# Kernel optimization log

Hardware: AMD Instinct MI355X
Metric: run time of the kernel (lower is better)

Reference implementation:

```python
import jax, jax.numpy as jnp
import numpy as np

N_NODES = 100000
N_EDGES = 400000
N_GRAPHS = 2500
DIM = 128
F_IN = 78
N_LAYERS = 3
BN_EPS = 1e-5


def setup_inputs() -> dict:
    key = jax.random.key(0)
    ks = jax.random.split(key, 24)
    def lin(k, fi, fo):
        return jax.random.normal(k, (fi, fo), jnp.float32) / np.sqrt(fi)
    inp = {
        "x": jax.random.normal(ks[0], (N_NODES, F_IN), jnp.float32),
        "edge_index": jax.random.randint(ks[1], (2, N_EDGES), 0, N_NODES, jnp.int32),
        "batch": jnp.sort(jax.random.randint(ks[2], (N_NODES,), 0, N_GRAPHS, jnp.int32)),
        "num_graphs": N_GRAPHS,
        "gcn1_W": lin(ks[3], F_IN, DIM), "gcn1_b": jnp.zeros((DIM,), jnp.float32),
        "gcn2_W": lin(ks[4], DIM, DIM), "gcn2_b": jnp.zeros((DIM,), jnp.float32),
        "gin0_w1": lin(ks[5], F_IN, DIM), "gin0_b1": jnp.zeros((DIM,), jnp.float32),
        "gin0_w2": lin(ks[6], DIM, DIM), "gin0_b2": jnp.zeros((DIM,), jnp.float32),
        # layers 1..2 stacked (same 128->128 shapes)
        "gin_w1": jnp.stack([lin(ks[7], DIM, DIM), lin(ks[8], DIM, DIM)]),
        "gin_b1": jnp.zeros((2, DIM), jnp.float32),
        "gin_w2": jnp.stack([lin(ks[9], DIM, DIM), lin(ks[10], DIM, DIM)]),
        "gin_b2": jnp.zeros((2, DIM), jnp.float32),
        "bn_gamma": jnp.ones((N_LAYERS, DIM), jnp.float32),
        "bn_beta": jnp.zeros((N_LAYERS, DIM), jnp.float32),
    }
    return inp


def reference(x, edge_index, batch, num_graphs,
              gcn1_W, gcn1_b, gcn2_W, gcn2_b,
              gin0_w1, gin0_b1, gin0_w2, gin0_b2,
              gin_w1, gin_b1, gin_w2, gin_b2,
              bn_gamma, bn_beta):
    n = x.shape[0]
    src, dst = edge_index[0], edge_index[1]

    def gcn(h, W, b):
        # linear -> symmetric-normalized aggregation with self loops (PyG GCNConv)
        h = h @ W
        loop = jnp.arange(n, dtype=src.dtype)
        s = jnp.concatenate([src, loop])
        d = jnp.concatenate([dst, loop])
        deg = jax.ops.segment_sum(jnp.ones(s.shape[0], h.dtype), d, num_segments=n)
        dis = jax.lax.rsqrt(deg)  # deg >= 1 thanks to self loops
        norm = (dis[s] * dis[d])[:, None]
        return jax.ops.segment_sum(h[s] * norm, d, num_segments=n) + b

    def gin(h, w1, b1, w2, b2):
        # GINConv, eps=0: mlp(x + sum_{j->i} x_j)
        agg = jax.ops.segment_sum(h[src], dst, num_segments=n)
        z = jax.nn.relu((h + agg) @ w1 + b1)
        return z @ w2 + b2

    def bn(h, g, bt):
        mu = h.mean(0)
        var = ((h - mu) ** 2).mean(0)
        return (h - mu) * jax.lax.rsqrt(var + BN_EPS) * g + bt

    g1 = jax.nn.relu(gcn(x, gcn1_W, gcn1_b))
    g2 = jax.nn.relu(gcn(g1, gcn2_W, gcn2_b))
    g2a = g2 + g1
    g2m = g2 * g1

    h = x
    xs = []
    m = jnp.float32(1.0)
    e = jnp.float32(0.0)
    for i in range(N_LAYERS):
        if i == 0:
            h = gin(h, gin0_w1, gin0_b1, gin0_w2, gin0_b2)
        else:
            h = gin(h, gin_w1[i - 1], gin_b1[i - 1], gin_w2[i - 1], gin_b2[i - 1])
        h = bn(jax.nn.relu(h), bn_gamma[i], bn_beta[i])
        m = m * h
        e = e + h
        xs.append(h)

    rep = jnp.concatenate(xs + [m, e, g1, g2, g2a, g2m], axis=-1)  # [N, 9*DIM]
    return jax.ops.segment_max(rep, batch, num_segments=num_graphs)
```

## Files before the change

### kernel.cpp

```cpp
#include <hip/hip_runtime.h>
#include <math.h>

#define DIMC 128
#define FINC 78
#define REPW 1152
#define SCAN_TILE 1024

typedef __attribute__((ext_vector_type(8))) short short8x;
typedef __attribute__((ext_vector_type(4))) float f32x4;

__device__ inline float b2f(unsigned short u) {
    union { unsigned int i; float f; } v; v.i = ((unsigned int)u) << 16; return v.f;
}
__device__ inline unsigned short f2b(float f) {
    union { float f; unsigned int i; } v; v.f = f;
    unsigned int r = (v.i + 0x7FFFu + ((v.i >> 16) & 1u)) >> 16;
    return (unsigned short)r;
}
__device__ inline float pf2f(unsigned int u) {
    union { unsigned int i; float f; } hi, lo;
    hi.i = u & 0xFFFF0000u;
    lo.i = u << 16;
    return hi.f + lo.f;
}
__device__ inline unsigned int f2pf(float v) {
    unsigned short hi = f2b(v);
    unsigned short lo = f2b(v - b2f(hi));
    return ((unsigned int)hi << 16) | (unsigned int)lo;
}
__device__ inline void pfacc4(uint4 u, float* a) {
    a[0] += pf2f(u.x); a[1] += pf2f(u.y); a[2] += pf2f(u.z); a[3] += pf2f(u.w);
}


__global__ void k_fill_int(int* __restrict__ p, int v, int n) {
    int i = blockIdx.x * blockDim.x + threadIdx.x;
    if (i < n) p[i] = v;
}

__global__ void k_fill(float* __restrict__ p, float v, int n) {
    int i = blockIdx.x * blockDim.x + threadIdx.x;
    if (i < n) p[i] = v;
}

__global__ void k_count(const int* __restrict__ dst, int* __restrict__ cnt, int E) {
    int e = blockIdx.x * blockDim.x + threadIdx.x;
    if (e < E) atomicAdd(&cnt[dst[e]], 1);
}

__launch_bounds__(256)
__global__ void k_tilesum(const int* __restrict__ cnt, int* __restrict__ tileSum, int N) {
    __shared__ int red[256];
    int base = blockIdx.x * SCAN_TILE;
    int s = 0;
    for (int i = threadIdx.x; i < SCAN_TILE; i += 256) {
        int idx = base + i;
        if (idx < N) s += cnt[idx];
    }
    red[threadIdx.x] = s;
    __syncthreads();
    for (int d = 128; d > 0; d >>= 1) {
        if (threadIdx.x < d) red[threadIdx.x] += red[threadIdx.x + d];
        __syncthreads();
    }
    if (threadIdx.x == 0) tileSum[blockIdx.x] = red[0];
}

__launch_bounds__(256)
__global__ void k_tilescan(const int* __restrict__ tileSum, int* __restrict__ tileOff,
                           int* __restrict__ rowptr, int T, int N) {
    __shared__ int sh[256];
    int t = threadIdx.x;
    int orig = (t < T) ? tileSum[t] : 0;
    sh[t] = orig;
    __syncthreads();
    for (int d = 1; d < 256; d <<= 1) {
        int v = (t >= d) ? sh[t - d] : 0;
        __syncthreads();
        sh[t] += v;
        __syncthreads();
    }
    if (t < T) tileOff[t] = sh[t] - orig;
    if (t == 255) rowptr[N] = sh[255];
}

__launch_bounds__(256)
__global__ void k_tileemit(const int* __restrict__ cnt, const int* __restrict__ tileOff,
                           int* __restrict__ rowptr, int* __restrict__ cursor,
                           float* __restrict__ dis, int N) {
    __shared__ int sh[256];
    int t = threadIdx.x;
    int base = blockIdx.x * SCAN_TILE;
    int idx0 = base + t * 4;
    int v0 = 0, v1 = 0, v2 = 0, v3 = 0;
    if (idx0 + 3 < N) {
        int4 v = *(const int4*)(cnt + idx0);
        v0 = v.x; v1 = v.y; v2 = v.z; v3 = v.w;
    } else {
        if (idx0 + 0 < N) v0 = cnt[idx0 + 0];
        if (idx0 + 1 < N) v1 = cnt[idx0 + 1];
        if (idx0 + 2 < N) v2 = cnt[idx0 + 2];
        if (idx0 + 3 < N) v3 = cnt[idx0 + 3];
    }
    int s0 = v0, s1 = s0 + v1, s2 = s1 + v2, s3 = s2 + v3;
    sh[t] = s3;
    __syncthreads();
    for (int d = 1; d < 256; d <<= 1) {
        int v = (t >= d) ? sh[t - d] : 0;
        __syncthreads();
        sh[t] += v;
        __syncthreads();
    }
    int gbase = tileOff[blockIdx.x] + ((t == 0) ? 0 : sh[t - 1]);
    int ex[4] = {0, s0, s1, s2};
    int vv[4] = {v0, v1, v2, v3};
#pragma unroll
    for (int j = 0; j < 4; ++j) {
        int idx = idx0 + j;
        if (idx < N) {
            int r = gbase + ex[j];
            rowptr[idx] = r;
            cursor[idx] = r;
            dis[idx] = rsqrtf((float)vv[j] + 1.0f);
        }
    }
}

__global__ void k_scatter(const int* __restrict__ src, const int* __restrict__ dst,
                          int* __restrict__ cursor, int* __restrict__ col, int E) {
    int e = blockIdx.x * blockDim.x + threadIdx.x;
    if (e < E) {
        int pos = atomicAdd(&cursor[dst[e]], 1);
        col[pos] = src[e];
    }
}

__global__ void k_bounds(const int* __restrict__ batch, int* __restrict__ start, int N, int G) {
    int g = blockIdx.x * blockDim.x + threadIdx.x;
    if (g <= G) {
        int lo = 0, hi = N;
        while (lo < hi) { int mid = (lo + hi) >> 1; if (batch[mid] < g) lo = mid + 1; else hi = mid; }
        start[g] = lo;
    }
}


__global__ void k_cvt_x(const float* __restrict__ x, unsigned int* __restrict__ xpk, int N) {
    int i = blockIdx.x * blockDim.x + threadIdx.x;
    if (i < N * 96) {
        int n = i / 96, k = i - n * 96;
        float v = (k < FINC) ? x[(size_t)n * FINC + k] : 0.f;
        xpk[i] = f2pf(v);
    }
}

__global__ void k_cvt_w(const float* __restrict__ s0, const float* __restrict__ s1,
                        const float* __restrict__ s2, const float* __restrict__ s3,
                        const float* __restrict__ s4, const float* __restrict__ s5,
                        unsigned short* __restrict__ whi, unsigned short* __restrict__ wlo) {
    int my = blockIdx.y;
    const float* src; int Ksrc, KP; size_t dstoff;
    const size_t o96 = (size_t)128 * 96, o128 = (size_t)128 * 128;
    switch (my) {
        case 0: src = s0; Ksrc = 78;  KP = 96;  dstoff = 0; break;
        case 1: src = s1; Ksrc = 78;  KP = 96;  dstoff = o96; break;
        case 2: src = s2; Ksrc = 128; KP = 128; dstoff = 2 * o96; break;
        case 3: src = s3; Ksrc = 128; KP = 128; dstoff = 2 * o96 + o128; break;
        case 4: src = s4; Ksrc = 128; KP = 128; dstoff = 2 * o96 + 2 * o128; break;
        default: src = s5; Ksrc = 128; KP = 128; dstoff = 2 * o96 + 3 * o128; break;
    }
    int i = blockIdx.x * blockDim.x + threadIdx.x;
    if (i < 128 * KP) {
        int n = i / KP, k = i - n * KP;
        float v = (k < Ksrc) ? src[(size_t)k * DIMC + n] : 0.f;
        unsigned short hi = f2b(v);
        wlo[dstoff + i] = f2b(v - b2f(hi));
        whi[dstoff + i] = hi;
    }
}


__launch_bounds__(256)
__global__ void k_bn_w(const float* __restrict__ bnsum, const float* __restrict__ gamma,
                       const float* __restrict__ beta, const float* __restrict__ w1,
                       float* __restrict__ coef, unsigned short* __restrict__ whiO,
                       unsigned short* __restrict__ wloO, float* __restrict__ cbeta, float invN) {
    __shared__ float sS[128], sT[128], sC[256];
    int t = threadIdx.x;
    if (t < 128) {
        float mu  = bnsum[t] * invN;
        float var = bnsum[128 + t] * invN - mu * mu;
        float inv = rsqrtf(var + 1e-5f);
        float s = gamma[t] * inv;
        float sh = beta[t] - mu * s;
        coef[t] = s; coef[128 + t] = sh;
        sS[t] = s; sT[t] = sh;
    }
    __syncthreads();
    for (int i = t; i < 16384; i += 256) {
        int n = i >> 7, k = i & 127;
        float v = w1[(size_t)k * 128 + n] * sS[k];
        unsigned short hi = f2b(v);
        whiO[i] = hi;
        wloO[i] = f2b(v - b2f(hi));
    }
    int n = t & 127, half = t >> 7;
    float acc = 0.f;
    for (int k = half * 64; k < half * 64 + 64; ++k) acc = fmaf(sT[k], w1[(size_t)k * 128 + n], acc);
    sC[t] = acc;
    __syncthreads();
    if (t < 128) cbeta[t] = sC[t] + sC[t + 128];
}

__global__ void k_bn_coef(const float* __restrict__ bnsum, const float* __restrict__ gamma,
                          const float* __restrict__ beta, float* __restrict__ coef, float invN) {
    int c = threadIdx.x;
    float mu  = bnsum[c] * invN;
    float var = bnsum[128 + c] * invN - mu * mu;
    float inv = rsqrtf(var + 1e-5f);
    float s = gamma[c] * inv;
    coef[c] = s;
    coef[128 + c] = beta[c] - mu * s;
}


template<int KP>
__launch_bounds__(256)
__global__ void k_gemm_pf(const unsigned int* __restrict__ Apk,
                          const unsigned short* __restrict__ Whi,
                          const unsigned short* __restrict__ Wlo,
                          const float* __restrict__ bias,
                          const float* __restrict__ rowScale,
                          float* __restrict__ statsOut,
                          unsigned int* __restrict__ Cpk,
                          int N, int doRelu) {
    __shared__ unsigned short sAhi[4 * 66 * 8], sAlo[4 * 66 * 8];
    __shared__ unsigned short sBhi[4 * 130 * 8], sBlo[4 * 130 * 8];
    __shared__ float sStats[256];
    const int tid = threadIdx.x;
    const int row0 = blockIdx.x * 64;

    const int wave = tid >> 6;
    const int lane = tid & 63;
    const int lm = lane & 15, q = lane >> 4;
    const int wc = wave * 32;

    f32x4 acc[4][2];
#pragma unroll
    for (int a = 0; a < 4; ++a)
#pragma unroll
        for (int b = 0; b < 2; ++b) acc[a][b] = (f32x4){0.f, 0.f, 0.f, 0.f};

    for (int k0 = 0; k0 < KP; k0 += 32) {
        if (k0) __syncthreads();
        {
            int g = tid & 3, r = tid >> 2;
            int gr = row0 + r;
            uint4 h = make_uint4(0, 0, 0, 0), l = make_uint4(0, 0, 0, 0);
            if (gr < N) {
                const unsigned int* p = Apk + (size_t)gr * KP + k0 + g * 8;
                uint4 u0 = *(const uint4*)(p);
                uint4 u1 = *(const uint4*)(p + 4);
                h.x = (u0.x >> 16) | (u0.y & 0xFFFF0000u);
                l.x = (u0.x & 0xFFFFu) | (u0.y << 16);
                h.y = (u0.z >> 16) | (u0.w & 0xFFFF0000u);
                l.y = (u0.z & 0xFFFFu) | (u0.w << 16);
                h.z = (u1.x >> 16) | (u1.y & 0xFFFF0000u);
                l.z = (u1.x & 0xFFFFu) | (u1.y << 16);
                h.w = (u1.z >> 16) | (u1.w & 0xFFFF0000u);
                l.w = (u1.z & 0xFFFFu) | (u1.w << 16);
            }
            size_t la = ((size_t)g * 66 + r) * 8;
            *(uint4*)(sAhi + la) = h;
            *(uint4*)(sAlo + la) = l;
        }
        for (int s = tid; s < 512; s += 256) {
            int g = s & 3, n = s >> 2;
            size_t gb = (size_t)n * KP + k0 + g * 8;
            size_t la = ((size_t)g * 130 + n) * 8;
            *(uint4*)(sBhi + la) = *(const uint4*)(Whi + gb);
            *(uint4*)(sBlo + la) = *(const uint4*)(Wlo + gb);
        }
        __syncthreads();

        short8x ah[4], al[4], bh[2], bl[2];
#pragma unroll
        for (int rt = 0; rt < 4; ++rt) {
            size_t addr = ((size_t)q * 66 + rt * 16 + lm) * 8;
            ah[rt] = *(const short8x*)(sAhi + addr);
            al[rt] = *(const short8x*)(sAlo + addr);
        }
#pragma unroll
        for (int ct = 0; ct < 2; ++ct) {
            size_t addr = ((size_t)q * 130 + wc + ct * 16 + lm) * 8;
            bh[ct] = *(const short8x*)(sBhi + addr);
            bl[ct] = *(const short8x*)(sBlo + addr);
        }
#pragma unroll
        for (int rt = 0; rt < 4; ++rt)
#pragma unroll
            for (int ct = 0; ct < 2; ++ct) {
                acc[rt][ct] = __builtin_amdgcn_mfma_f32_16x16x32_bf16(ah[rt], bh[ct], acc[rt][ct], 0, 0, 0);
                acc[rt][ct] = __builtin_amdgcn_mfma_f32_16x16x32_bf16(ah[rt], bl[ct], acc[rt][ct], 0, 0, 0);
                acc[rt][ct] = __builtin_amdgcn_mfma_f32_16x16x32_bf16(al[rt], bh[ct], acc[rt][ct], 0, 0, 0);
            }
    }

    float cs[2] = {0.f, 0.f}, cq[2] = {0.f, 0.f};
#pragma unroll
    for (int rt = 0; rt < 4; ++rt) {
#pragma unroll
        for (int i = 0; i < 4; ++i) {
            int row = rt * 16 + q * 4 + i;
            int gr = row0 + row;
            if (gr < N) {
                float sc = rowScale ? rowScale[gr] : 1.f;
#pragma unroll
                for (int ct = 0; ct < 2; ++ct) {
                    int colg = wc + ct * 16 + lm;
                    float v = acc[rt][ct][i];
                    if (bias) v += bias[colg];
                    if (doRelu) v = fmaxf(v, 0.f);
                    v *= sc;
                    Cpk[(size_t)gr * DIMC + colg] = f2pf(v);
                    if (statsOut) { cs[ct] += v; cq[ct] = fmaf(v, v, cq[ct]); }
                }
            }
        }
    }
    if (statsOut) {
        sStats[tid] = 0.f;
        __syncthreads();
#pragma unroll
        for (int ct = 0; ct < 2; ++ct) {
            int colg = wc + ct * 16 + lm;
            atomicAdd(&sStats[colg], cs[ct]);
            atomicAdd(&sStats[128 + colg], cq[ct]);
        }
        __syncthreads();
        atomicAdd(&statsOut[tid], sStats[tid]);
    }
}


__global__ void k_gather_gcn_pf(const unsigned int* __restrict__ t, const int* __restrict__ rowptr,
                                const int* __restrict__ col, const float* __restrict__ dis,
                                const float* __restrict__ bias, unsigned int* __restrict__ out, int N) {
    int i = blockIdx.x * blockDim.x + threadIdx.x;
    int node = i >> 5, c4 = (i & 31) * 4;
    if (node >= N) return;
    int s = rowptr[node], e = rowptr[node + 1];
    float acc[4] = {0.f, 0.f, 0.f, 0.f};
    pfacc4(*(const uint4*)(t + (size_t)node * DIMC + c4), acc);
    int k = s;
    for (; k + 1 < e; k += 2) {
        uint4 v0 = *(const uint4*)(t + (size_t)col[k] * DIMC + c4);
        uint4 v1 = *(const uint4*)(t + (size_t)col[k + 1] * DIMC + c4);
        pfacc4(v0, acc);
        pfacc4(v1, acc);
    }
    if (k < e) pfacc4(*(const uint4*)(t + (size_t)col[k] * DIMC + c4), acc);
    float d = dis[node];
    uint4 r;
    r.x = f2pf(fmaxf(acc[0] * d + bias[c4 + 0], 0.f));
    r.y = f2pf(fmaxf(acc[1] * d + bias[c4 + 1], 0.f));
    r.z = f2pf(fmaxf(acc[2] * d + bias[c4 + 2], 0.f));
    r.w = f2pf(fmaxf(acc[3] * d + bias[c4 + 3], 0.f));
    *(uint4*)(out + (size_t)node * DIMC + c4) = r;
}

__global__ void k_gather_gin_pf(const unsigned int* __restrict__ t, const int* __restrict__ rowptr,
                                const int* __restrict__ col, const float* __restrict__ bias,
                                const float* __restrict__ cbeta, unsigned int* __restrict__ out, int N) {
    int i = blockIdx.x * blockDim.x + threadIdx.x;
    int node = i >> 5, c4 = (i & 31) * 4;
    if (node >= N) return;
    int s = rowptr[node], e = rowptr[node + 1];
    float acc[4] = {0.f, 0.f, 0.f, 0.f};
    pfacc4(*(const uint4*)(t + (size_t)node * DIMC + c4), acc);
    int k = s;
    for (; k + 1 < e; k += 2) {
        uint4 v0 = *(const uint4*)(t + (size_t)col[k] * DIMC + c4);
        uint4 v1 = *(const uint4*)(t + (size_t)col[k + 1] * DIMC + c4);
        pfacc4(v0, acc);
        pfacc4(v1, acc);
    }
    if (k < e) pfacc4(*(const uint4*)(t + (size_t)col[k] * DIMC + c4), acc);
    float deg1 = (float)(e - s + 1);
    uint4 r;
#pragma unroll
    for (int j = 0; j < 4; ++j) {
        float v = acc[j] + bias[c4 + j];
        if (cbeta) v = fmaf(deg1, cbeta[c4 + j], v);
        ((unsigned int*)&r)[j] = f2pf(fmaxf(v, 0.f));
    }
    *(uint4*)(out + (size_t)node * DIMC + c4) = r;
}


__global__ void k_segmax_gin_all(const unsigned int* __restrict__ h0, const unsigned int* __restrict__ h1,
                                 const unsigned int* __restrict__ h2, const float* __restrict__ coef,
                                 const int* __restrict__ start, float* __restrict__ out) {
    int g = blockIdx.x, c = threadIdx.x;
    float s0 = coef[c],       t0 = coef[128 + c];
    float s1 = coef[256 + c], t1 = coef[384 + c];
    float s2 = coef[512 + c], t2 = coef[640 + c];
    int s = start[g], e = start[g + 1];
    float m0 = -INFINITY, m1 = -INFINITY, m2 = -INFINITY, mm = -INFINITY, me = -INFINITY;
    for (int n = s; n < e; ++n) {
        size_t idx = (size_t)n * DIMC + c;
        float a0 = fmaf(pf2f(h0[idx]), s0, t0);
        float a1 = fmaf(pf2f(h1[idx]), s1, t1);
        float a2 = fmaf(pf2f(h2[idx]), s2, t2);
        m0 = fmaxf(m0, a0); m1 = fmaxf(m1, a1); m2 = fmaxf(m2, a2);
        mm = fmaxf(mm, a0 * a1 * a2);
        me = fmaxf(me, a0 + a1 + a2);
    }
    size_t o = (size_t)g * REPW + c;
    out[o]            = m0;
    out[o + 1 * DIMC] = m1;
    out[o + 2 * DIMC] = m2;
    out[o + 3 * DIMC] = mm;
    out[o + 4 * DIMC] = me;
}

__global__ void k_segmax_gcn(const unsigned int* __restrict__ G1, const unsigned int* __restrict__ G2,
                             const int* __restrict__ start, float* __restrict__ out) {
    int g = blockIdx.x, c = threadIdx.x;
    int s = start[g], e = start[g + 1];
    float m1 = -INFINITY, m2 = -INFINITY, ma = -INFINITY, mm = -INFINITY;
    for (int n = s; n < e; ++n) {
        size_t idx = (size_t)n * DIMC + c;
        float a = pf2f(G1[idx]);
        float b = pf2f(G2[idx]);
        m1 = fmaxf(m1, a); m2 = fmaxf(m2, b);
        ma = fmaxf(ma, a + b); mm = fmaxf(mm, a * b);
    }
    size_t o = (size_t)g * REPW + c;
    out[o + 5 * DIMC] = m1;
    out[o + 6 * DIMC] = m2;
    out[o + 7 * DIMC] = ma;
    out[o + 8 * DIMC] = mm;
}


extern "C" void kernel_launch(void* const* d_in, const int* in_sizes, int n_in,
                              void* d_out, int out_size, void* d_ws, size_t ws_size,
                              hipStream_t stream) {
    const float* x       = (const float*)d_in[0];
    const int*   ei      = (const int*)d_in[1];
    const int*   batch   = (const int*)d_in[2];
    const float* gcn1_W  = (const float*)d_in[4];
    const float* gcn1_b  = (const float*)d_in[5];
    const float* gcn2_W  = (const float*)d_in[6];
    const float* gcn2_b  = (const float*)d_in[7];
    const float* gin0_w1 = (const float*)d_in[8];
    const float* gin0_b1 = (const float*)d_in[9];
    const float* gin0_w2 = (const float*)d_in[10];
    const float* gin0_b2 = (const float*)d_in[11];
    const float* gin_w1  = (const float*)d_in[12];
    const float* gin_b1  = (const float*)d_in[13];
    const float* gin_w2  = (const float*)d_in[14];
    const float* gin_b2  = (const float*)d_in[15];
    const float* bn_g    = (const float*)d_in[16];
    const float* bn_b    = (const float*)d_in[17];
    float* out = (float*)d_out;

    const int N = in_sizes[0] / FINC;
    const int E = in_sizes[1] / 2;
    const int G = out_size / REPW;
    const int* srcv = ei;
    const int* dstv = ei + E;

    auto cdiv = [](long a, long b) { return (int)((a + b - 1) / b); };
    const int gemmGrid = cdiv(N, 64);

    char* ws = (char*)d_ws;
    size_t off = 0;
    auto alloc = [&](size_t bytes) { char* p = ws + off; off += (bytes + 255) & ~(size_t)255; return p; };
    int*   cnt     = (int*)alloc(N * 4);
    int*   rowptr  = (int*)alloc((N + 1) * 4);
    int*   cursor  = (int*)alloc(N * 4);
    int*   col     = (int*)alloc(E * 4);
    float* dis     = (float*)alloc(N * 4);
    float* bnsum   = (float*)alloc(768 * 4);
    float* coef    = (float*)alloc(768 * 4);
    float* cbeta   = (float*)alloc(128 * 4);
    int*   start   = (int*)alloc((G + 1) * 4);
    int*   tileSum = (int*)alloc(256 * 4);
    int*   tileOff = (int*)alloc(256 * 4);
    const size_t wtElems = 2 * (size_t)128 * 96 + 4 * (size_t)128 * 128;
    unsigned short* whi = (unsigned short*)alloc(wtElems * 2);
    unsigned short* wlo = (unsigned short*)alloc(wtElems * 2);
    unsigned short* w1shi = (unsigned short*)alloc((size_t)128 * 128 * 2);
    unsigned short* w1slo = (unsigned short*)alloc((size_t)128 * 128 * 2);
    const size_t P = (size_t)N * DIMC;
    unsigned int* tT = (unsigned int*)alloc(P * 4);
    unsigned int* z  = (unsigned int*)alloc(P * 4);
    unsigned int* h0 = (unsigned int*)alloc(P * 4);
    unsigned int* h1 = (unsigned int*)alloc(P * 4);
    unsigned int* h2 = (unsigned int*)alloc(P * 4);
    unsigned int* xpk = h2;
    (void)ws_size; (void)n_in;

    const size_t o96 = (size_t)128 * 96, o128 = (size_t)128 * 128;
    const size_t woff[6] = {0, o96, 2 * o96, 2 * o96 + o128, 2 * o96 + 2 * o128, 2 * o96 + 3 * o128};

    const int T = 256;
    const int gatherGrid = cdiv((long)N * 32, T);
    const int nTiles = cdiv(N, SCAN_TILE);
    const float invN = 1.0f / (float)N;

    k_fill_int<<<cdiv(N, T), T, 0, stream>>>(cnt, 0, N);
    k_count<<<cdiv(E, T), T, 0, stream>>>(dstv, cnt, E);
    k_tilesum<<<nTiles, T, 0, stream>>>(cnt, tileSum, N);
    k_tilescan<<<1, T, 0, stream>>>(tileSum, tileOff, rowptr, nTiles, N);
    k_tileemit<<<nTiles, T, 0, stream>>>(cnt, tileOff, rowptr, cursor, dis, N);
    k_scatter<<<cdiv(E, T), T, 0, stream>>>(srcv, dstv, cursor, col, E);
    k_bounds<<<cdiv(G + 1, T), T, 0, stream>>>(batch, start, N, G);
    k_fill<<<3, T, 0, stream>>>(bnsum, 0.f, 768);
    k_cvt_x<<<cdiv((long)N * 96, T), T, 0, stream>>>(x, xpk, N);
    {
        dim3 g(64, 6);
        k_cvt_w<<<g, T, 0, stream>>>(gcn1_W, gin0_w1, gcn2_W, gin0_w2,
                                     gin_w2, gin_w2 + o128, whi, wlo);
    }

    k_gemm_pf<96><<<gemmGrid, T, 0, stream>>>(xpk, whi + woff[0], wlo + woff[0],
                                              nullptr, dis, nullptr, tT, N, 0);
    k_gather_gcn_pf<<<gatherGrid, T, 0, stream>>>(tT, rowptr, col, dis, gcn1_b, h1, N);
    k_gemm_pf<128><<<gemmGrid, T, 0, stream>>>(h1, whi + woff[2], wlo + woff[2],
                                               nullptr, dis, nullptr, tT, N, 0);
    k_gather_gcn_pf<<<gatherGrid, T, 0, stream>>>(tT, rowptr, col, dis, gcn2_b, z, N);
    k_segmax_gcn<<<G, DIMC, 0, stream>>>(h1, z, start, out);

    k_gemm_pf<96><<<gemmGrid, T, 0, stream>>>(xpk, whi + woff[1], wlo + woff[1],
                                              nullptr, nullptr, nullptr, tT, N, 0);
    k_gather_gin_pf<<<gatherGrid, T, 0, stream>>>(tT, rowptr, col, gin0_b1, nullptr, z, N);
    k_gemm_pf<128><<<gemmGrid, T, 0, stream>>>(z, whi + woff[3], wlo + woff[3],
                                               gin0_b2, nullptr, bnsum, h0, N, 1);

    const unsigned int* hsrc[2] = {h0, h1};
    unsigned int* hdst[2] = {h1, h2};
    for (int L = 1; L <= 2; ++L) {
        k_bn_w<<<1, T, 0, stream>>>(bnsum + (L - 1) * 256, bn_g + (L - 1) * DIMC, bn_b + (L - 1) * DIMC,
                                    gin_w1 + (size_t)(L - 1) * o128, coef + (L - 1) * 256,
                                    w1shi, w1slo, cbeta, invN);
        k_gemm_pf<128><<<gemmGrid, T, 0, stream>>>(hsrc[L - 1], w1shi, w1slo,
                                                   nullptr, nullptr, nullptr, tT, N, 0);
        k_gather_gin_pf<<<gatherGrid, T, 0, stream>>>(tT, rowptr, col,
                                                      gin_b1 + (size_t)(L - 1) * DIMC, cbeta, z, N);
        k_gemm_pf<128><<<gemmGrid, T, 0, stream>>>(z, whi + woff[3 + L], wlo + woff[3 + L],
                                                   gin_b2 + (size_t)(L - 1) * DIMC, nullptr,
                                                   bnsum + L * 256, hdst[L - 1], N, 1);
    }
    k_bn_coef<<<1, DIMC, 0, stream>>>(bnsum + 512, bn_g + 2 * DIMC, bn_b + 2 * DIMC, coef + 512, invN);

    k_segmax_gin_all<<<G, DIMC, 0, stream>>>(h0, h1, h2, coef, start, out);
}
```

Measured before the change: 812.0 us.

## Prefetch all A chunks into registers and stage full weight matrix in LDS

The GEMM kernel now issues every global load for its A rows up front, holding them in registers, and copies the whole B (weight hi/lo) matrix into shared memory once before the K loop. Previously each 32-wide K chunk waited on its own global loads. The intent is to hide global memory latency and remove the per-chunk B reloads. In exchange it uses more registers and more shared memory (NG*130*8*2 shorts for B), which can lower occupancy.

```diff
diff --git a/kernel.cpp b/kernel.cpp
--- a/kernel.cpp
+++ b/kernel.cpp
@@ -234,8 +234,10 @@
                           float* __restrict__ statsOut,
                           unsigned int* __restrict__ Cpk,
                           int N, int doRelu) {
+    constexpr int NCH = KP / 32;
+    constexpr int NG  = KP / 8;
     __shared__ unsigned short sAhi[4 * 66 * 8], sAlo[4 * 66 * 8];
-    __shared__ unsigned short sBhi[4 * 130 * 8], sBlo[4 * 130 * 8];
+    __shared__ unsigned short sBhi[NG * 130 * 8], sBlo[NG * 130 * 8];
     __shared__ float sStats[256];
     const int tid = threadIdx.x;
     const int row0 = blockIdx.x * 64;
@@ -245,41 +247,51 @@
     const int lm = lane & 15, q = lane >> 4;
     const int wc = wave * 32;
 
+    const int ag = tid & 3, ar = tid >> 2;
+    const int agr = row0 + ar;
+    uint4 apre[2 * NCH];
+    if (agr < N) {
+        const unsigned int* p = Apk + (size_t)agr * KP + ag * 8;
+#pragma unroll
+        for (int c = 0; c < NCH; ++c) {
+            apre[2 * c]     = *(const uint4*)(p + c * 32);
+            apre[2 * c + 1] = *(const uint4*)(p + c * 32 + 4);
+        }
+    } else {
+#pragma unroll
+        for (int c = 0; c < 2 * NCH; ++c) apre[c] = make_uint4(0, 0, 0, 0);
+    }
+
+    for (int s = tid; s < NG * 128; s += 256) {
+        int g = s >> 7, n = s & 127;
+        size_t gb = (size_t)n * KP + g * 8;
+        size_t la = ((size_t)g * 130 + n) * 8;
+        *(uint4*)(sBhi + la) = *(const uint4*)(Whi + gb);
+        *(uint4*)(sBlo + la) = *(const uint4*)(Wlo + gb);
+    }
+
     f32x4 acc[4][2];
 #pragma unroll
     for (int a = 0; a < 4; ++a)
 #pragma unroll
         for (int b = 0; b < 2; ++b) acc[a][b] = (f32x4){0.f, 0.f, 0.f, 0.f};
 
-    for (int k0 = 0; k0 < KP; k0 += 32) {
-        if (k0) __syncthreads();
+#pragma unroll
+    for (int c = 0; c < NCH; ++c) {
         {
-            int g = tid & 3, r = tid >> 2;
-            int gr = row0 + r;
-            uint4 h = make_uint4(0, 0, 0, 0), l = make_uint4(0, 0, 0, 0);
-            if (gr < N) {
-                const unsigned int* p = Apk + (size_t)gr * KP + k0 + g * 8;
-                uint4 u0 = *(const uint4*)(p);
-                uint4 u1 = *(const uint4*)(p + 4);
-                h.x = (u0.x >> 16) | (u0.y & 0xFFFF0000u);
-                l.x = (u0.x & 0xFFFFu) | (u0.y << 16);
-                h.y = (u0.z >> 16) | (u0.w & 0xFFFF0000u);
-                l.y = (u0.z & 0xFFFFu) | (u0.w << 16);
-                h.z = (u1.x >> 16) | (u1.y & 0xFFFF0000u);
-                l.z = (u1.x & 0xFFFFu) | (u1.y << 16);
-                h.w = (u1.z >> 16) | (u1.w & 0xFFFF0000u);
-                l.w = (u1.z & 0xFFFFu) | (u1.w << 16);
-            }
-            size_t la = ((size_t)g * 66 + r) * 8;
+            uint4 u0 = apre[2 * c], u1 = apre[2 * c + 1];
+            uint4 h, l;
+            h.x = (u0.x >> 16) | (u0.y & 0xFFFF0000u);
+            l.x = (u0.x & 0xFFFFu) | (u0.y << 16);
+            h.y = (u0.z >> 16) | (u0.w & 0xFFFF0000u);
+            l.y = (u0.z & 0xFFFFu) | (u0.w << 16);
+            h.z = (u1.x >> 16) | (u1.y & 0xFFFF0000u);
+            l.z = (u1.x & 0xFFFFu) | (u1.y << 16);
+            h.w = (u1.z >> 16) | (u1.w & 0xFFFF0000u);
+            l.w = (u1.z & 0xFFFFu) | (u1.w << 16);
+            size_t la = ((size_t)ag * 66 + ar) * 8;
             *(uint4*)(sAhi + la) = h;
             *(uint4*)(sAlo + la) = l;
-        }
-        for (int s = tid; s < 512; s += 256) {
-            int g = s & 3, n = s >> 2;
-            size_t gb = (size_t)n * KP + k0 + g * 8;
-            size_t la = ((size_t)g * 130 + n) * 8;
-            *(uint4*)(sBhi + la) = *(const uint4*)(Whi + gb);
-            *(uint4*)(sBlo + la) = *(const uint4*)(Wlo + gb);
         }
         __syncthreads();
 
@@ -292,7 +304,7 @@
         }
 #pragma unroll
         for (int ct = 0; ct < 2; ++ct) {
-            size_t addr = ((size_t)q * 130 + wc + ct * 16 + lm) * 8;
+            size_t addr = ((size_t)(c * 4 + q) * 130 + wc + ct * 16 + lm) * 8;
             bh[ct] = *(const short8x*)(sBhi + addr);
             bl[ct] = *(const short8x*)(sBlo + addr);
         }
@@ -304,6 +316,7 @@
                 acc[rt][ct] = __builtin_amdgcn_mfma_f32_16x16x32_bf16(ah[rt], bl[ct], acc[rt][ct], 0, 0, 0);
                 acc[rt][ct] = __builtin_amdgcn_mfma_f32_16x16x32_bf16(al[rt], bh[ct], acc[rt][ct], 0, 0, 0);
             }
+        if (c + 1 < NCH) __syncthreads();
     }
 
     float cs[2] = {0.f, 0.f}, cq[2] = {0.f, 0.f};
```

After: 957.9 us. 18.0% more time.
